# Optimization experiments

Hardware: AMD Instinct MI355X
Metric: run time of the kernel (lower is better)

Reference implementation:

```python
import jax, jax.numpy as jnp
import numpy as np

B, S, HID = 1, 4096, 2048
H, KV, D = 16, 8, 128
N_REP = H // KV
SCALING = float(128 ** -0.5)   # query_pre_attn_scalar ** -0.5
SOFTCAP = 50.0
WINDOW = 1024
NEG = -1e9


def setup_inputs() -> dict:
    key = jax.random.key(0)
    ks = jax.random.split(key, 6)
    hidden_states = jax.random.normal(ks[0], (B, S, HID), dtype=jnp.float32)
    Wq = jax.random.normal(ks[1], (HID, H * D), dtype=jnp.float32) * 0.02
    Wk = jax.random.normal(ks[2], (HID, KV * D), dtype=jnp.float32) * 0.02
    Wv = jax.random.normal(ks[3], (HID, KV * D), dtype=jnp.float32) * 0.02
    Wo = jax.random.normal(ks[4], (H * D, HID), dtype=jnp.float32) * 0.02
    # RoPE tables [1, S, D]
    inv_freq = 1.0 / (10000.0 ** (jnp.arange(0, D, 2, dtype=jnp.float32) / D))
    freqs = jnp.outer(jnp.arange(S, dtype=jnp.float32), inv_freq)   # [S, D/2]
    emb = jnp.concatenate([freqs, freqs], axis=-1)                  # [S, D]
    cos = jnp.cos(emb)[None]
    sin = jnp.sin(emb)[None]
    # causal + sliding-window additive mask [1, 1, S, S]
    i = jnp.arange(S)[:, None]
    j = jnp.arange(S)[None, :]
    allowed = (j <= i) & ((i - j) < WINDOW)
    attention_mask = jnp.where(allowed, 0.0, NEG).astype(jnp.float32)[None, None]
    return {"hidden_states": hidden_states, "cos": cos, "sin": sin,
            "attention_mask": attention_mask, "Wq": Wq, "Wk": Wk, "Wv": Wv, "Wo": Wo}


def _rotate_half(x):
    x1, x2 = jnp.split(x, 2, axis=-1)
    return jnp.concatenate([-x2, x1], axis=-1)


def reference(hidden_states, cos, sin, attention_mask, Wq, Wk, Wv, Wo):
    b, s, _ = hidden_states.shape
    # projections -> [B, heads, S, D]
    q = (hidden_states @ Wq).reshape(b, s, H, D).transpose(0, 2, 1, 3)
    k = (hidden_states @ Wk).reshape(b, s, KV, D).transpose(0, 2, 1, 3)
    v = (hidden_states @ Wv).reshape(b, s, KV, D).transpose(0, 2, 1, 3)
    # RoPE (unsqueeze_dim=1)
    c = cos[:, None]  # [B, 1, S, D]
    sn = sin[:, None]
    q = q * c + _rotate_half(q) * sn
    k = k * c + _rotate_half(k) * sn
    # repeat_kv (GQA)
    k = jnp.repeat(k, N_REP, axis=1)
    v = jnp.repeat(v, N_REP, axis=1)
    # scores with softcap + mask
    scores = jnp.einsum('bhqd,bhkd->bhqk', q, k) * SCALING
    scores = jnp.tanh(scores / SOFTCAP) * SOFTCAP
    scores = scores + attention_mask
    attn = jax.nn.softmax(scores.astype(jnp.float32), axis=-1).astype(q.dtype)
    out = jnp.einsum('bhqk,bhkd->bhqd', attn, v)
    out = out.transpose(0, 2, 1, 3).reshape(b, s, H * D)
    return out @ Wo
```

## Files before the change

kernel.cpp:

```cpp
#include <hip/hip_runtime.h>

#define S 4096
#define HID 2048
#define NH 16
#define NKV 8
#define HD 128
#define WINDOW 1024
#define SCALING 0.08838834764831845f
#define SOFTCAP 50.0f

typedef __bf16 bf16x8 __attribute__((ext_vector_type(8)));
typedef __bf16 bf16x4 __attribute__((ext_vector_type(4)));
typedef float f32x4 __attribute__((ext_vector_type(4)));

__device__ inline void gll16(const void* g, void* l) {
  __builtin_amdgcn_global_load_lds((const __attribute__((address_space(1))) void*)g,
                                   (__attribute__((address_space(3))) void*)l, 16, 0, 0);
}

__global__ void prep_all(const float* __restrict__ hs, __bf16* __restrict__ hsb,
                         const float* __restrict__ Wq, const float* __restrict__ Wk,
                         const float* __restrict__ Wv, const float* __restrict__ Wo,
                         __bf16* __restrict__ wqkvT, __bf16* __restrict__ woT) {
  int b = blockIdx.x;
  int t = threadIdx.x;
  if (b < 8192) {
    int i = b * 256 + t;
    float4 v = ((const float4*)hs)[i];
    bf16x4 o;
    o[0] = (__bf16)v.x; o[1] = (__bf16)v.y; o[2] = (__bf16)v.z; o[3] = (__bf16)v.w;
    ((bf16x4*)hsb)[i] = o;
    return;
  }
  __shared__ float tile[64][65];
  int y = b - 8192;
  int k0 = (y & 31) * 64;
  int wy = y >> 5;
  const float* src; __bf16* dst; int Nsrc, c0, perm, n0;
  if (wy < 32)      { src = Wq; dst = wqkvT; Nsrc = 2048; c0 = wy * 64;        perm = 1; n0 = wy * 64; }
  else if (wy < 48) { src = Wk; dst = wqkvT; Nsrc = 1024; c0 = (wy - 32) * 64; perm = 1; n0 = 2048 + (wy - 32) * 64; }
  else if (wy < 64) { src = Wv; dst = wqkvT; Nsrc = 1024; c0 = (wy - 48) * 64; perm = 0; n0 = 3072 + (wy - 48) * 64; }
  else              { src = Wo; dst = woT;   Nsrc = 2048; c0 = (wy - 64) * 64; perm = 0; n0 = (wy - 64) * 64; }
#pragma unroll
  for (int e = 0; e < 16; ++e) {
    int f = e * 256 + t; int r = f >> 6, c = f & 63;
    tile[r][c] = src[(size_t)(k0 + r) * Nsrc + c0 + c];
  }
  __syncthreads();
#pragma unroll
  for (int e = 0; e < 16; ++e) {
    int f = e * 256 + t; int r = f >> 6, c = f & 63;
    int n = n0 + r;
    if (perm) {
      int d = n & 127, o = d >> 4;
      int g = (o < 4) ? (o * 2) : ((o - 4) * 2 + 1);
      n = (n & ~127) | (g << 4) | (d & 15);
    }
    dst[(size_t)n * 2048 + k0 + c] = (__bf16)tile[c][r];
  }
}

__global__ __launch_bounds__(256) void gemm_qkv(const __bf16* __restrict__ A,
                                                const __bf16* __restrict__ B,
                                                __bf16* __restrict__ qr,
                                                __bf16* __restrict__ kr,
                                                __bf16* __restrict__ vt,
                                                const float* __restrict__ cosp,
                                                const float* __restrict__ sinp) {
  __shared__ __align__(16) __bf16 As[128 * 64];
  __shared__ __align__(16) __bf16 Bs[128 * 64];
  const int K = 2048;
  int m0 = blockIdx.x * 128, n0 = blockIdx.y * 128;
  int t = threadIdx.x;
  int lane = t & 63, wave = t >> 6;
  int wm = wave & 1, wn = wave >> 1;
  int quad = lane >> 4, l16 = lane & 15;

  f32x4 acc[4][4] = {};

  const __bf16* Abase = A + (size_t)m0 * K;
  const __bf16* Bbase = B + (size_t)n0 * K;

  for (int kk = 0; kk < K; kk += 64) {
    __syncthreads();
#pragma unroll
    for (int i = 0; i < 4; ++i) {
      int idx = i * 256 + t;
      int row = idx >> 3, c = idx & 7;
      int g = (c ^ (row & 7)) * 8;
      gll16(Abase + (size_t)row * K + kk + g, &As[idx * 8]);
      gll16(Bbase + (size_t)row * K + kk + g, &Bs[idx * 8]);
    }
    __syncthreads();
#pragma unroll
    for (int ks = 0; ks < 64; ks += 32) {
      bf16x8 af[4], bfr[4];
#pragma unroll
      for (int i = 0; i < 4; ++i) {
        int row = wm * 64 + i * 16 + l16;
        af[i] = *(const bf16x8*)&As[row * 64 + (((quad + (ks >> 3)) ^ (row & 7)) * 8)];
      }
#pragma unroll
      for (int j = 0; j < 4; ++j) {
        int row = wn * 64 + j * 16 + l16;
        bfr[j] = *(const bf16x8*)&Bs[row * 64 + (((quad + (ks >> 3)) ^ (row & 7)) * 8)];
      }
#pragma unroll
      for (int i = 0; i < 4; ++i)
#pragma unroll
        for (int j = 0; j < 4; ++j)
          acc[i][j] = __builtin_amdgcn_mfma_f32_16x16x32_bf16(af[i], bfr[j], acc[i][j], 0, 0, 0);
    }
  }

  if (n0 < 3072) {
    __bf16* dst = (n0 < 2048) ? (qr + (size_t)(n0 >> 7) * S * 128)
                              : (kr + (size_t)((n0 - 2048) >> 7) * S * 128);
#pragma unroll
    for (int i = 0; i < 4; ++i)
#pragma unroll
      for (int r = 0; r < 4; ++r) {
        int row = m0 + wm * 64 + i * 16 + quad * 4 + r;
#pragma unroll
        for (int jp = 0; jp < 2; ++jp) {
          int ifr = (wn * 2 + jp) * 16 + l16;
          float c = cosp[(size_t)row * 128 + ifr];
          float sn = sinp[(size_t)row * 128 + ifr];
          float lo = acc[i][2 * jp][r], hi = acc[i][2 * jp + 1][r];
          dst[(size_t)row * 128 + wn * 64 + jp * 32 + l16]      = (__bf16)(lo * c - hi * sn);
          dst[(size_t)row * 128 + wn * 64 + jp * 32 + 16 + l16] = (__bf16)(hi * c + lo * sn);
        }
      }
  } else {
    int vc0 = n0 - 3072;
#pragma unroll
    for (int i = 0; i < 4; ++i)
#pragma unroll
      for (int j = 0; j < 4; ++j) {
        int row_base = m0 + wm * 64 + i * 16 + quad * 4;
        int col = vc0 + wn * 64 + j * 16 + l16;
        bf16x4 ov;
#pragma unroll
        for (int r = 0; r < 4; ++r) ov[r] = (__bf16)acc[i][j][r];
        *(bf16x4*)&vt[(size_t)col * S + row_base] = ov;
      }
  }
}

template <typename OutT>
__global__ __launch_bounds__(256) void gemm_bt(const __bf16* __restrict__ A,
                                               const __bf16* __restrict__ B,
                                               OutT* __restrict__ C, int N, int K) {
  __shared__ __align__(16) __bf16 As[128 * 64];
  __shared__ __align__(16) __bf16 Bs[128 * 64];
  int m0 = blockIdx.x * 128, n0 = blockIdx.y * 128;
  int t = threadIdx.x;
  int lane = t & 63, wave = t >> 6;
  int wm = wave & 1, wn = wave >> 1;
  int quad = lane >> 4, l16 = lane & 15;

  f32x4 acc[4][4] = {};

  const __bf16* Abase = A + (size_t)m0 * K;
  const __bf16* Bbase = B + (size_t)n0 * K;

  for (int kk = 0; kk < K; kk += 64) {
    __syncthreads();
#pragma unroll
    for (int i = 0; i < 4; ++i) {
      int idx = i * 256 + t;
      int row = idx >> 3, c = idx & 7;
      int g = (c ^ (row & 7)) * 8;
      gll16(Abase + (size_t)row * K + kk + g, &As[idx * 8]);
      gll16(Bbase + (size_t)row * K + kk + g, &Bs[idx * 8]);
    }
    __syncthreads();
#pragma unroll
    for (int ks = 0; ks < 64; ks += 32) {
      bf16x8 af[4], bfr[4];
#pragma unroll
      for (int i = 0; i < 4; ++i) {
        int row = wm * 64 + i * 16 + l16;
        af[i] = *(const bf16x8*)&As[row * 64 + (((quad + (ks >> 3)) ^ (row & 7)) * 8)];
      }
#pragma unroll
      for (int j = 0; j < 4; ++j) {
        int row = wn * 64 + j * 16 + l16;
        bfr[j] = *(const bf16x8*)&Bs[row * 64 + (((quad + (ks >> 3)) ^ (row & 7)) * 8)];
      }
#pragma unroll
      for (int i = 0; i < 4; ++i)
#pragma unroll
        for (int j = 0; j < 4; ++j)
          acc[i][j] = __builtin_amdgcn_mfma_f32_16x16x32_bf16(af[i], bfr[j], acc[i][j], 0, 0, 0);
    }
  }
#pragma unroll
  for (int i = 0; i < 4; ++i)
#pragma unroll
    for (int j = 0; j < 4; ++j)
#pragma unroll
      for (int r = 0; r < 4; ++r) {
        int row = m0 + wm * 64 + i * 16 + quad * 4 + r;
        int col = n0 + wn * 64 + j * 16 + l16;
        C[(size_t)row * N + col] = (OutT)acc[i][j][r];
      }
}

__global__ __launch_bounds__(512) void attn(const __bf16* __restrict__ qr,
                                            const __bf16* __restrict__ kr,
                                            const __bf16* __restrict__ vt,
                                            __bf16* __restrict__ ao) {
  __shared__ __align__(16) __bf16 Ks[2][64 * 128];
  __shared__ __align__(16) __bf16 Vs[3][128 * 64];

  int kvh = blockIdx.x;
  int q0 = blockIdx.y * 128;
  int t = threadIdx.x, lane = t & 63, wave = t >> 6;
  int quad = lane >> 4, l16 = lane & 15;
  int h = kvh * 2 + (wave & 1);
  int qbase = q0 + (wave >> 1) * 32;

  bf16x8 qf[2][4];
#pragma unroll
  for (int mi = 0; mi < 2; ++mi) {
    const __bf16* qptr = qr + ((size_t)h * S + qbase + mi * 16 + l16) * 128;
#pragma unroll
    for (int ks = 0; ks < 4; ++ks)
      qf[mi][ks] = *(const bf16x8*)&qptr[ks * 32 + quad * 8];
  }

  f32x4 o[2][8] = {};
  float lpart[2] = {0.f, 0.f};

  int lo = q0 - (WINDOW - 1); if (lo < 0) lo = 0;
  int kt_begin = (lo / 64) * 64;
  int kt_end = q0 + 128;
  int NT = (kt_end - kt_begin) >> 6;

  const __bf16* kbase0 = kr + (size_t)kvh * S * 128;
  const __bf16* vbase0 = vt + (size_t)kvh * 128 * S;

  float4 kreg[2];
  float2 vregA[2], vregB[2];

  auto load_regs = [&](int kt) {
    const __bf16* kb = kbase0 + (size_t)kt * 128;
    const __bf16* vb = vbase0 + kt;
#pragma unroll
    for (int i = 0; i < 2; ++i) {
      int off = i * 512 + t;
      kreg[i] = *(const float4*)(kb + (size_t)off * 8);
      int r = off >> 3, c = off & 7;
      int base0 = 32 * (c >> 2) + 4 * (c & 3);
      vregA[i] = *(const float2*)(vb + (size_t)r * S + base0);
      vregB[i] = *(const float2*)(vb + (size_t)r * S + base0 + 16);
    }
  };
  auto write_lds = [&](int kslot, int vslot) {
#pragma unroll
    for (int i = 0; i < 2; ++i) {
      int off = i * 512 + t;
      { int r = off >> 4, c = off & 15;
        *(float4*)&Ks[kslot][r * 128 + ((c ^ (r & 15)) * 8)] = kreg[i]; }
      { int r = off >> 3, c = off & 7;
        float4 v = {vregA[i].x, vregA[i].y, vregB[i].x, vregB[i].y};
        *(float4*)&Vs[vslot][r * 64 + ((c ^ (r & 7)) * 8)] = v; }
    }
  };

  const float XS = SCALING / SOFTCAP;
  f32x4 sA[2][4], sB[2][4];

  auto activ = [&](int kt0) {
    return !(kt0 > qbase + 31 || kt0 + 63 < qbase - (WINDOW - 1));
  };

  auto step = [&](int tt, f32x4 (&SC)[2][4], f32x4 (&SP)[2][4], int vr, int vw) {
    if (tt < NT) {
      int kt0 = kt_begin + tt * 64;
      if (activ(kt0)) {
        int kslot = tt & 1;
#pragma unroll
        for (int mi = 0; mi < 2; ++mi)
#pragma unroll
          for (int nt = 0; nt < 4; ++nt) SC[mi][nt] = {};
        __builtin_amdgcn_s_setprio(1);
#pragma unroll
        for (int nt = 0; nt < 4; ++nt) {
#pragma unroll
          for (int ks = 0; ks < 4; ++ks) {
            bf16x8 kf = *(const bf16x8*)&Ks[kslot][(nt * 16 + l16) * 128 + (((ks * 4 + quad) ^ l16) * 8)];
            SC[0][nt] = __builtin_amdgcn_mfma_f32_16x16x32_bf16(kf, qf[0][ks], SC[0][nt], 0, 0, 0);
            SC[1][nt] = __builtin_amdgcn_mfma_f32_16x16x32_bf16(kf, qf[1][ks], SC[1][nt], 0, 0, 0);
          }
        }
        __builtin_amdgcn_s_setprio(0);
      }
    }

    if (tt > 0) {
      int kt0c = kt_begin + (tt - 1) * 64;
      if (activ(kt0c)) {
        bf16x4 pk[2][4];
        bool interior = (kt0c + 63 <= qbase) && (kt0c >= qbase + 31 - (WINDOW - 1));
#pragma unroll
        for (int mi = 0; mi < 2; ++mi) {
          int irow = qbase + mi * 16 + l16;
#pragma unroll
          for (int nt = 0; nt < 4; ++nt)
#pragma unroll
            for (int r = 0; r < 4; ++r) {
              float x = SP[mi][nt][r] * XS;
              x = fminf(fmaxf(x, -0.25f), 0.25f);
              float x2 = x * x;
              float th = x * fmaf(x2, fmaf(x2, 0.13333333f, -0.33333333f), 1.0f);
              float pp = __builtin_amdgcn_exp2f(fmaf(th, 72.134752f, -72.134752f));
              if (!interior) {
                int j = kt0c + nt * 16 + quad * 4 + r;
                bool ok = (j <= irow) && (irow - j < WINDOW);
                pp = ok ? pp : 0.0f;
              }
              lpart[mi] += pp;
              pk[mi][nt][r] = (__bf16)pp;
            }
        }

        bf16x8 pB[2][2];
#pragma unroll
        for (int mi = 0; mi < 2; ++mi)
#pragma unroll
          for (int ks = 0; ks < 2; ++ks)
#pragma unroll
            for (int e = 0; e < 4; ++e) {
              pB[mi][ks][e]     = pk[mi][2 * ks][e];
              pB[mi][ks][4 + e] = pk[mi][2 * ks + 1][e];
            }

        __builtin_amdgcn_s_setprio(1);
#pragma unroll
        for (int dt = 0; dt < 8; ++dt) {
          int row = dt * 16 + l16;
#pragma unroll
          for (int ks = 0; ks < 2; ++ks) {
            bf16x8 vf = *(const bf16x8*)&Vs[vr][row * 64 + (((ks * 4 + quad) ^ (l16 & 7)) * 8)];
#pragma unroll
            for (int mi = 0; mi < 2; ++mi)
              o[mi][dt] = __builtin_amdgcn_mfma_f32_16x16x32_bf16(vf, pB[mi][ks], o[mi][dt], 0, 0, 0);
          }
        }
        __builtin_amdgcn_s_setprio(0);
      }
    }

    if (tt + 1 < NT) write_lds((tt + 1) & 1, vw);
    if (tt + 2 < NT) load_regs(kt_begin + (tt + 2) * 64);
    __syncthreads();
  };

  load_regs(kt_begin);
  write_lds(0, 0);
  if (NT > 1) load_regs(kt_begin + 64);
  __syncthreads();

  int vw = 1, vr = 2;
  for (int tt = 0; tt < NT; tt += 2) {
    step(tt, sA, sB, vr, vw);
    if (++vw == 3) vw = 0; if (++vr == 3) vr = 0;
    step(tt + 1, sB, sA, vr, vw);
    if (++vw == 3) vw = 0; if (++vr == 3) vr = 0;
  }
  step(NT, sA, sB, vr, vw);

#pragma unroll
  for (int mi = 0; mi < 2; ++mi) {
    float ls = lpart[mi];
    ls += __shfl_xor(ls, 16);
    ls += __shfl_xor(ls, 32);
    float inv = 1.f / ls;
    int row = qbase + mi * 16 + l16;
    __bf16* dst = ao + (size_t)row * (NH * HD) + h * HD + quad * 4;
#pragma unroll
    for (int dt = 0; dt < 8; ++dt) {
      bf16x4 ov;
#pragma unroll
      for (int r = 0; r < 4; ++r) ov[r] = (__bf16)(o[mi][dt][r] * inv);
      *(bf16x4*)(dst + dt * 16) = ov;
    }
  }
}

extern "C" void kernel_launch(void* const* d_in, const int* in_sizes, int n_in,
                              void* d_out, int out_size, void* d_ws, size_t ws_size,
                              hipStream_t stream) {
  const float* hs   = (const float*)d_in[0];
  const float* cosp = (const float*)d_in[1];
  const float* sinp = (const float*)d_in[2];
  const float* Wq = (const float*)d_in[4];
  const float* Wk = (const float*)d_in[5];
  const float* Wv = (const float*)d_in[6];
  const float* Wo = (const float*)d_in[7];
  float* out = (float*)d_out;

  char* w = (char*)d_ws;
  __bf16* hsb   = (__bf16*)w; w += (size_t)S * HID * 2;
  __bf16* wqkvT = (__bf16*)w; w += (size_t)4096 * 2048 * 2;
  __bf16* woT   = (__bf16*)w; w += (size_t)2048 * 2048 * 2;
  __bf16* qr    = (__bf16*)w; w += (size_t)NH * S * HD * 2;
  __bf16* kr    = (__bf16*)w; w += (size_t)NKV * S * HD * 2;
  __bf16* vtb   = (__bf16*)w; w += (size_t)NKV * HD * S * 2;
  __bf16* ao    = (__bf16*)w; w += (size_t)S * 2048 * 2;

  prep_all<<<8192 + 3072, 256, 0, stream>>>(hs, hsb, Wq, Wk, Wv, Wo, wqkvT, woT);

  gemm_qkv<<<dim3(32, 32), 256, 0, stream>>>(hsb, wqkvT, qr, kr, vtb, cosp, sinp);

  attn<<<dim3(NKV, 32), 512, 0, stream>>>(qr, kr, vtb, ao);

  gemm_bt<float><<<dim3(32, 16), 256, 0, stream>>>(ao, woT, out, 2048, 2048);
}
```

Measured before the change: 358.1 us.

## Deepen attention software pipeline to three stages with four-slot V buffer

```diff
diff --git a/kernel.cpp b/kernel.cpp
--- a/kernel.cpp
+++ b/kernel.cpp
@@ -212,7 +212,7 @@
                                             const __bf16* __restrict__ vt,
                                             __bf16* __restrict__ ao) {
   __shared__ __align__(16) __bf16 Ks[2][64 * 128];
-  __shared__ __align__(16) __bf16 Vs[3][128 * 64];
+  __shared__ __align__(16) __bf16 Vs[4][128 * 64];
 
   int kvh = blockIdx.x;
   int q0 = blockIdx.y * 128;
@@ -271,89 +271,90 @@
 
   const float XS = SCALING / SOFTCAP;
   f32x4 sA[2][4], sB[2][4];
-
-  auto activ = [&](int kt0) {
+  bf16x8 pbA[2][2], pbB[2][2];
+
+  auto activ = [&](int tt) {
+    int kt0 = kt_begin + tt * 64;
     return !(kt0 > qbase + 31 || kt0 + 63 < qbase - (WINDOW - 1));
   };
 
-  auto step = [&](int tt, f32x4 (&SC)[2][4], f32x4 (&SP)[2][4], int vr, int vw) {
-    if (tt < NT) {
-      int kt0 = kt_begin + tt * 64;
-      if (activ(kt0)) {
-        int kslot = tt & 1;
+  auto do_qk = [&](int tt, f32x4 (&SC)[2][4]) {
+    if (tt >= NT || !activ(tt)) return;
+    int kslot = tt & 1;
+#pragma unroll
+    for (int mi = 0; mi < 2; ++mi)
+#pragma unroll
+      for (int nt = 0; nt < 4; ++nt) SC[mi][nt] = {};
+    __builtin_amdgcn_s_setprio(1);
+#pragma unroll
+    for (int nt = 0; nt < 4; ++nt) {
+#pragma unroll
+      for (int ks = 0; ks < 4; ++ks) {
+        bf16x8 kf = *(const bf16x8*)&Ks[kslot][(nt * 16 + l16) * 128 + (((ks * 4 + quad) ^ l16) * 8)];
+        SC[0][nt] = __builtin_amdgcn_mfma_f32_16x16x32_bf16(kf, qf[0][ks], SC[0][nt], 0, 0, 0);
+        SC[1][nt] = __builtin_amdgcn_mfma_f32_16x16x32_bf16(kf, qf[1][ks], SC[1][nt], 0, 0, 0);
+      }
+    }
+    __builtin_amdgcn_s_setprio(0);
+  };
+
+  auto do_pv = [&](int tt, bf16x8 (&PB)[2][2]) {
+    if (tt < 0 || tt >= NT || !activ(tt)) return;
+    int vr = tt & 3;
+    __builtin_amdgcn_s_setprio(1);
+#pragma unroll
+    for (int dt = 0; dt < 8; ++dt) {
+      int row = dt * 16 + l16;
+#pragma unroll
+      for (int ks = 0; ks < 2; ++ks) {
+        bf16x8 vf = *(const bf16x8*)&Vs[vr][row * 64 + (((ks * 4 + quad) ^ (l16 & 7)) * 8)];
 #pragma unroll
         for (int mi = 0; mi < 2; ++mi)
-#pragma unroll
-          for (int nt = 0; nt < 4; ++nt) SC[mi][nt] = {};
-        __builtin_amdgcn_s_setprio(1);
-#pragma unroll
-        for (int nt = 0; nt < 4; ++nt) {
-#pragma unroll
-          for (int ks = 0; ks < 4; ++ks) {
-            bf16x8 kf = *(const bf16x8*)&Ks[kslot][(nt * 16 + l16) * 128 + (((ks * 4 + quad) ^ l16) * 8)];
-            SC[0][nt] = __builtin_amdgcn_mfma_f32_16x16x32_bf16(kf, qf[0][ks], SC[0][nt], 0, 0, 0);
-            SC[1][nt] = __builtin_amdgcn_mfma_f32_16x16x32_bf16(kf, qf[1][ks], SC[1][nt], 0, 0, 0);
+          o[mi][dt] = __builtin_amdgcn_mfma_f32_16x16x32_bf16(vf, PB[mi][ks], o[mi][dt], 0, 0, 0);
+      }
+    }
+    __builtin_amdgcn_s_setprio(0);
+  };
+
+  auto do_sm = [&](int tt, f32x4 (&SP)[2][4], bf16x8 (&PB)[2][2]) {
+    if (tt < 0 || tt >= NT || !activ(tt)) return;
+    int kt0c = kt_begin + tt * 64;
+    bf16x4 pk[2][4];
+    bool interior = (kt0c + 63 <= qbase) && (kt0c >= qbase + 31 - (WINDOW - 1));
+#pragma unroll
+    for (int mi = 0; mi < 2; ++mi) {
+      int irow = qbase + mi * 16 + l16;
+#pragma unroll
+      for (int nt = 0; nt < 4; ++nt)
+#pragma unroll
+        for (int r = 0; r < 4; ++r) {
+          float x = SP[mi][nt][r] * XS;
+          x = fminf(fmaxf(x, -0.25f), 0.25f);
+          float x2 = x * x;
+          float th = x * fmaf(x2, fmaf(x2, 0.13333333f, -0.33333333f), 1.0f);
+          float pp = __builtin_amdgcn_exp2f(fmaf(th, 72.134752f, -72.134752f));
+          if (!interior) {
+            int j = kt0c + nt * 16 + quad * 4 + r;
+            bool ok = (j <= irow) && (irow - j < WINDOW);
+            pp = ok ? pp : 0.0f;
           }
+          lpart[mi] += pp;
+          pk[mi][nt][r] = (__bf16)pp;
         }
-        __builtin_amdgcn_s_setprio(0);
-      }
-    }
-
-    if (tt > 0) {
-      int kt0c = kt_begin + (tt - 1) * 64;
-      if (activ(kt0c)) {
-        bf16x4 pk[2][4];
-        bool interior = (kt0c + 63 <= qbase) && (kt0c >= qbase + 31 - (WINDOW - 1));
-#pragma unroll
-        for (int mi = 0; mi < 2; ++mi) {
-          int irow = qbase + mi * 16 + l16;
-#pragma unroll
-          for (int nt = 0; nt < 4; ++nt)
-#pragma unroll
-            for (int r = 0; r < 4; ++r) {
-              float x = SP[mi][nt][r] * XS;
-              x = fminf(fmaxf(x, -0.25f), 0.25f);
-              float x2 = x * x;
-              float th = x * fmaf(x2, fmaf(x2, 0.13333333f, -0.33333333f), 1.0f);
-              float pp = __builtin_amdgcn_exp2f(fmaf(th, 72.134752f, -72.134752f));
-              if (!interior) {
-                int j = kt0c + nt * 16 + quad * 4 + r;
-                bool ok = (j <= irow) && (irow - j < WINDOW);
-                pp = ok ? pp : 0.0f;
-              }
-              lpart[mi] += pp;
-              pk[mi][nt][r] = (__bf16)pp;
-            }
+    }
+#pragma unroll
+    for (int mi = 0; mi < 2; ++mi)
+#pragma unroll
+      for (int ks = 0; ks < 2; ++ks)
+#pragma unroll
+        for (int e = 0; e < 4; ++e) {
+          PB[mi][ks][e]     = pk[mi][2 * ks][e];
+          PB[mi][ks][4 + e] = pk[mi][2 * ks + 1][e];
         }
-
-        bf16x8 pB[2][2];
-#pragma unroll
-        for (int mi = 0; mi < 2; ++mi)
-#pragma unroll
-          for (int ks = 0; ks < 2; ++ks)
-#pragma unroll
-            for (int e = 0; e < 4; ++e) {
-              pB[mi][ks][e]     = pk[mi][2 * ks][e];
-              pB[mi][ks][4 + e] = pk[mi][2 * ks + 1][e];
-            }
-
-        __builtin_amdgcn_s_setprio(1);
-#pragma unroll
-        for (int dt = 0; dt < 8; ++dt) {
-          int row = dt * 16 + l16;
-#pragma unroll
-          for (int ks = 0; ks < 2; ++ks) {
-            bf16x8 vf = *(const bf16x8*)&Vs[vr][row * 64 + (((ks * 4 + quad) ^ (l16 & 7)) * 8)];
-#pragma unroll
-            for (int mi = 0; mi < 2; ++mi)
-              o[mi][dt] = __builtin_amdgcn_mfma_f32_16x16x32_bf16(vf, pB[mi][ks], o[mi][dt], 0, 0, 0);
-          }
-        }
-        __builtin_amdgcn_s_setprio(0);
-      }
-    }
-
-    if (tt + 1 < NT) write_lds((tt + 1) & 1, vw);
+  };
+
+  auto stage_step = [&](int tt) {
+    if (tt + 1 < NT) write_lds((tt + 1) & 1, (tt + 1) & 3);
     if (tt + 2 < NT) load_regs(kt_begin + (tt + 2) * 64);
     __syncthreads();
   };
@@ -363,14 +364,19 @@
   if (NT > 1) load_regs(kt_begin + 64);
   __syncthreads();
 
-  int vw = 1, vr = 2;
   for (int tt = 0; tt < NT; tt += 2) {
-    step(tt, sA, sB, vr, vw);
-    if (++vw == 3) vw = 0; if (++vr == 3) vr = 0;
-    step(tt + 1, sB, sA, vr, vw);
-    if (++vw == 3) vw = 0; if (++vr == 3) vr = 0;
-  }
-  step(NT, sA, sB, vr, vw);
+    do_qk(tt, sA);
+    do_pv(tt - 2, pbA);
+    do_sm(tt - 1, sB, pbB);
+    stage_step(tt);
+    do_qk(tt + 1, sB);
+    do_pv(tt - 1, pbB);
+    do_sm(tt, sA, pbA);
+    stage_step(tt + 1);
+  }
+  do_pv(NT - 2, pbA);
+  do_sm(NT - 1, sB, pbB);
+  do_pv(NT - 1, pbB);
 
 #pragma unroll
   for (int mi = 0; mi < 2; ++mi) {
@@ -409,7 +415,7 @@
   __bf16* qr    = (__bf16*)w; w += (size_t)NH * S * HD * 2;
   __bf16* kr    = (__bf16*)w; w += (size_t)NKV * S * HD * 2;
   __bf16* vtb   = (__bf16*)w; w += (size_t)NKV * HD * S * 2;
-  __bf16* ao    = (__bf16*)w; w += (size_t)S * 2048 * 2;
+  __bf16* ao    = hsb;
 
   prep_all<<<8192 + 3072, 256, 0, stream>>>(hs, hsb, Wq, Wk, Wv, Wo, wqkvT, woT);
 
```

Result: slower. 377.4 us (+5.4%).
